# Optimization experiments

Measured on AMD Instinct MI355X. Metric: run time of the kernel, lower is better.

The kernel has to match this reference:

```python
import jax, jax.numpy as jnp
import numpy as np

K = 5       # local window size (odd)
G = 4       # groups

def _gconv1x1(x, w):
    # grouped 1x1 conv: x (b,c,h,w), w (g, c_out_g, c_in_g) -> (b,g,c_out_g,h,w)
    b, c, h, wd = x.shape
    g, co, ci = w.shape
    xg = x.reshape(b, g, ci, h, wd)
    return jnp.einsum('bgihw,goi->bgohw', xg, w)

def _windows(f, h, w):
    # f: (b,g,n,h+2p,w+2p) -> (b,g,n,h,w,K*K), row-major over (ki,kj)
    # matches torch .unfold(2,K,1).unfold(3,K,1).view(..., -1)
    return jnp.stack([f[..., i:i + h, j:j + w]
                      for i in range(K) for j in range(K)], axis=-1)

def setup_inputs() -> dict:
    key = jax.random.key(0)
    k1, k2, k3, k4 = jax.random.split(key, 4)
    x = jax.random.normal(k1, (2, 128, 96, 96), dtype=jnp.float32)
    wq = jax.random.normal(k2, (G, 32, 32), dtype=jnp.float32) * 0.1
    wk = jax.random.normal(k3, (G, 32, 32), dtype=jnp.float32) * 0.1
    wv = jax.random.normal(k4, (G, 32, 32), dtype=jnp.float32) * 0.1
    return {"x": x, "wq": wq, "wk": wk, "wv": wv}

def reference(x, wq, wk, wv):
    b, c, h, w = x.shape
    p = K // 2
    # query: plain grouped 1x1 conv, broadcast over window dim
    q = _gconv1x1(x, wq)[..., None]                      # (b,g,n,h,w,1)
    # key/value: reflect-pad (1x1 conv commutes with padding, same as torch's
    # Conv2d(..., padding=k//2, padding_mode='reflect'))
    xp = jnp.pad(x, ((0, 0), (0, 0), (p, p), (p, p)), mode='reflect')
    kf = _gconv1x1(xp, wk)                               # (b,g,n,h+2p,w+2p)
    vf = _gconv1x1(xp, wv)
    kwin = _windows(kf, h, w)                            # (b,g,n,h,w,K*K)
    vwin = _windows(vf, h, w)
    attn = jax.nn.softmax(q * kwin, axis=-1)             # per-channel window softmax
    y = (attn * vwin).sum(-1)                            # (b,g,n,h,w)
    return y.reshape(b, -1, h, w)                        # (b, c_out, h, w)
```

## Files before the change

### kernel.cpp

```cpp
#include <hip/hip_runtime.h>


#define HW 96
#define RG 12
#define NPOS 144
#define KVSTR 145

typedef short short8 __attribute__((ext_vector_type(8)));
typedef float float4v __attribute__((ext_vector_type(4)));

__device__ __forceinline__ int refl(int i) {
    i = (i < 0) ? -i : i;
    i = (i > 95) ? (190 - i) : i;
    return i;
}

__device__ __forceinline__ unsigned int bfr(float f) {
    return (__float_as_uint(f) + 0x8000u) >> 16;
}

__global__ __launch_bounds__(256) void fused_attn(
    const float* __restrict__ x, const float* __restrict__ wq,
    const float* __restrict__ wk, const float* __restrict__ wv,
    float* __restrict__ out)
{
    __shared__ unsigned short xs[NPOS * 32];
    __shared__ unsigned int   kvb[32 * KVSTR];
    __shared__ unsigned short qs[32 * 64];

    const int tid = threadIdx.x;
    const int g = blockIdx.y, b = blockIdx.z;
    const int h0 = (blockIdx.x / 12) * 8;
    const int w0 = (blockIdx.x % 12) * 8;
    const float* xg = x + (size_t)(b * 128 + g * 32) * (HW * HW);

    const int wA   = min(max(w0 - 4, 0), 80);
    const int colB = wA - w0 + 2;
    #pragma unroll
    for (int it = 0; it < 6; it++) {
        int idx = it * 256 + tid;
        int seg = idx & 3;
        int pr  = idx >> 2;
        int ch  = pr & 31;
        int row = pr >> 5;
        int iy  = refl(h0 + row - 2);
        const float4v f4 = *(const float4v*)(xg + ch * (HW * HW) + iy * HW + wA + seg * 4);
        int col0 = colB + seg * 4;
        #pragma unroll
        for (int e = 0; e < 4; e++) {
            int col = col0 + e;
            if (col >= 0 && col < RG)
                xs[(row * RG + col) * 32 + ch] = (unsigned short)bfr(f4[e]);
        }
    }

    const int wid  = tid >> 6;
    const int lane = tid & 63;
    const int n0   = wid * 8;
    const int col  = lane & 15;
    const int quad = lane >> 4;
    const int koff = quad * 8;

    const float* wrow = (col < 8) ? (wk + (g * 32 + n0 + col) * 32)
                                  : (wv + (g * 32 + n0 + col - 8) * 32);
    short8 bkv;
    #pragma unroll
    for (int j = 0; j < 8; j++)
        ((unsigned short*)&bkv)[j] = (unsigned short)bfr(wrow[koff + j]);

    short8 bq = {0, 0, 0, 0, 0, 0, 0, 0};
    if (col < 8) {
        const float* qr = wq + (g * 32 + n0 + col) * 32;
        #pragma unroll
        for (int j = 0; j < 8; j++)
            ((unsigned short*)&bq)[j] = (unsigned short)bfr(qr[koff + j]);
    }

    if (w0 == 0 || w0 == 88) {
        __syncthreads();
        const int left = (w0 == 0);
        for (int it = 0; it < 3; it++) {
            int idx = it * 256 + tid;
            int ch  = idx & 31;
            int rr  = idx >> 5;
            int row = rr >> 1, wc = rr & 1;
            int dstc = left ? wc : (10 + wc);
            int srcc = left ? (4 - wc) : (8 - wc);
            xs[(row * RG + dstc) * 32 + ch] = xs[(row * RG + srcc) * 32 + ch];
        }
    }
    __syncthreads();

    #pragma unroll
    for (int t = 0; t < 9; t++) {
        int p = t * 16 + col;
        short8 a = *(const short8*)&xs[p * 32 + koff];
        float4v d = {0.f, 0.f, 0.f, 0.f};
        d = __builtin_amdgcn_mfma_f32_16x16x32_bf16(a, bkv, d, 0, 0, 0);
        int c = n0 + (col & 7);
        unsigned short* dst0 = (unsigned short*)&kvb[c * KVSTR + t * 16 + quad * 4];
        int half = (col < 8) ? 0 : 1;
        #pragma unroll
        for (int r = 0; r < 4; r++)
            dst0[2 * r + half] = (unsigned short)bfr(d[r]);
    }

    #pragma unroll
    for (int t = 0; t < 4; t++) {
        int mp = t * 16 + col;
        int p  = ((mp >> 3) + 2) * RG + (mp & 7) + 2;
        short8 a = *(const short8*)&xs[p * 32 + koff];
        float4v d = {0.f, 0.f, 0.f, 0.f};
        d = __builtin_amdgcn_mfma_f32_16x16x32_bf16(a, bq, d, 0, 0, 0);
        if (col < 8) {
            unsigned int* dst = (unsigned int*)&qs[(n0 + col) * 64 + t * 16 + quad * 4];
            unsigned int u0 = __float_as_uint(d[0]) + 0x8000u;
            unsigned int u1 = __float_as_uint(d[1]) + 0x8000u;
            unsigned int u2 = __float_as_uint(d[2]) + 0x8000u;
            unsigned int u3 = __float_as_uint(d[3]) + 0x8000u;
            dst[0] = __builtin_amdgcn_perm(u1, u0, 0x07060302);
            dst[1] = __builtin_amdgcn_perm(u3, u2, 0x07060302);
        }
    }

    __syncthreads();

    const int ty = lane >> 3, tx = lane & 7;
    float* outp = out + (size_t)((b * 128 + g * 32 + n0) * HW + (h0 + ty)) * HW + (w0 + tx);
    for (int n = 0; n < 8; n++) {
        int c = n0 + n;
        float q = __uint_as_float((unsigned int)qs[c * 64 + lane] << 16) * 1.44269504f;
        float den = 0.f, num = 0.f;
        #pragma unroll
        for (int dy = 0; dy < 5; dy++) {
            const unsigned int* rowp = &kvb[c * KVSTR + (ty + dy) * RG + tx];
            #pragma unroll
            for (int dx = 0; dx < 5; dx++) {
                unsigned int u = rowp[dx];
                float kf = __uint_as_float(u << 16);
                float vf = __uint_as_float(u & 0xffff0000u);
                float e;
                asm("v_exp_f32 %0, %1" : "=v"(e) : "v"(q * kf));
                den += e;
                num = fmaf(e, vf, num);
            }
        }
        outp[n * (HW * HW)] = num * __builtin_amdgcn_rcpf(den);
    }
}

extern "C" void kernel_launch(void* const* d_in, const int* in_sizes, int n_in,
                              void* d_out, int out_size, void* d_ws, size_t ws_size,
                              hipStream_t stream) {
    const float* x  = (const float*)d_in[0];
    const float* wq = (const float*)d_in[1];
    const float* wk = (const float*)d_in[2];
    const float* wv = (const float*)d_in[3];
    float* out = (float*)d_out;

    dim3 grid(144, 4, 2);
    fused_attn<<<grid, 256, 0, stream>>>(x, wq, wk, wv, out);
}
```

Measured before the change: 93.61 us.

## Transpose KV shared layout to position-major and process two channels per iteration

```diff
diff --git a/kernel.cpp b/kernel.cpp
--- a/kernel.cpp
+++ b/kernel.cpp
@@ -4,10 +4,16 @@
 #define HW 96
 #define RG 12
 #define NPOS 144
-#define KVSTR 145
+#define CSTR 33
 
 typedef short short8 __attribute__((ext_vector_type(8)));
 typedef float float4v __attribute__((ext_vector_type(4)));
+
+#if __has_builtin(__builtin_amdgcn_exp2f)
+#define EXP2(x) __builtin_amdgcn_exp2f(x)
+#else
+#define EXP2(x) __expf((x) * 0.6931471805599453f)
+#endif
 
 __device__ __forceinline__ int refl(int i) {
     i = (i < 0) ? -i : i;
@@ -25,7 +31,7 @@
     float* __restrict__ out)
 {
     __shared__ unsigned short xs[NPOS * 32];
-    __shared__ unsigned int   kvb[32 * KVSTR];
+    __shared__ unsigned int   kvb[NPOS * CSTR];
     __shared__ unsigned short qs[32 * 64];
 
     const int tid = threadIdx.x;
@@ -91,18 +97,20 @@
     }
     __syncthreads();
 
+    unsigned short* kv16 = (unsigned short*)kvb;
     #pragma unroll
     for (int t = 0; t < 9; t++) {
-        int p = t * 16 + col;
-        short8 a = *(const short8*)&xs[p * 32 + koff];
+        int pa = t * 16 + col;
+        short8 a = *(const short8*)&xs[pa * 32 + koff];
         float4v d = {0.f, 0.f, 0.f, 0.f};
         d = __builtin_amdgcn_mfma_f32_16x16x32_bf16(a, bkv, d, 0, 0, 0);
-        int c = n0 + (col & 7);
-        unsigned short* dst0 = (unsigned short*)&kvb[c * KVSTR + t * 16 + quad * 4];
-        int half = (col < 8) ? 0 : 1;
+        int c    = n0 + (col & 7);
+        int half = col >> 3;
         #pragma unroll
-        for (int r = 0; r < 4; r++)
-            dst0[2 * r + half] = (unsigned short)bfr(d[r]);
+        for (int r = 0; r < 4; r++) {
+            int p = t * 16 + quad * 4 + r;
+            kv16[(p * CSTR + c) * 2 + half] = (unsigned short)bfr(d[r]);
+        }
     }
 
     #pragma unroll
@@ -127,25 +135,32 @@
 
     const int ty = lane >> 3, tx = lane & 7;
     float* outp = out + (size_t)((b * 128 + g * 32 + n0) * HW + (h0 + ty)) * HW + (w0 + tx);
-    for (int n = 0; n < 8; n++) {
-        int c = n0 + n;
-        float q = __uint_as_float((unsigned int)qs[c * 64 + lane] << 16) * 1.44269504f;
-        float den = 0.f, num = 0.f;
+    for (int j = 0; j < 4; j++) {
+        int c0 = n0 + 2 * j;
+        float q0 = __uint_as_float((unsigned int)qs[c0 * 64 + lane] << 16) * 1.44269504f;
+        float q1 = __uint_as_float((unsigned int)qs[(c0 + 1) * 64 + lane] << 16) * 1.44269504f;
+        float den0 = 0.f, num0 = 0.f, den1 = 0.f, num1 = 0.f;
         #pragma unroll
         for (int dy = 0; dy < 5; dy++) {
-            const unsigned int* rowp = &kvb[c * KVSTR + (ty + dy) * RG + tx];
+            const unsigned int* rowp = &kvb[((ty + dy) * RG + tx) * CSTR + c0];
+            float rd0 = 0.f, rn0 = 0.f, rd1 = 0.f, rn1 = 0.f;
             #pragma unroll
             for (int dx = 0; dx < 5; dx++) {
-                unsigned int u = rowp[dx];
-                float kf = __uint_as_float(u << 16);
-                float vf = __uint_as_float(u & 0xffff0000u);
-                float e;
-                asm("v_exp_f32 %0, %1" : "=v"(e) : "v"(q * kf));
-                den += e;
-                num = fmaf(e, vf, num);
+                unsigned int u0 = rowp[dx * CSTR];
+                unsigned int u1 = rowp[dx * CSTR + 1];
+                float k0 = __uint_as_float(u0 << 16);
+                float v0 = __uint_as_float(u0 & 0xffff0000u);
+                float k1 = __uint_as_float(u1 << 16);
+                float v1 = __uint_as_float(u1 & 0xffff0000u);
+                float e0 = EXP2(q0 * k0);
+                float e1 = EXP2(q1 * k1);
+                rd0 += e0; rn0 = fmaf(e0, v0, rn0);
+                rd1 += e1; rn1 = fmaf(e1, v1, rn1);
             }
+            den0 += rd0; num0 += rn0; den1 += rd1; num1 += rn1;
         }
-        outp[n * (HW * HW)] = num * __builtin_amdgcn_rcpf(den);
+        outp[(2 * j)     * (HW * HW)] = num0 * __builtin_amdgcn_rcpf(den0);
+        outp[(2 * j + 1) * (HW * HW)] = num1 * __builtin_amdgcn_rcpf(den1);
     }
 }
 
```

After: 94.86 us. No clear change (+1.3%).

## Switch to fp16 MFMA, channel-innermost K/V layout, vectorized window loads

Applied to the files above, without the earlier changes.

```diff
diff --git a/kernel.cpp b/kernel.cpp
--- a/kernel.cpp
+++ b/kernel.cpp
@@ -4,10 +4,12 @@
 #define HW 96
 #define RG 12
 #define NPOS 144
-#define KVSTR 145
+#define CSTR 36
 
-typedef short short8 __attribute__((ext_vector_type(8)));
-typedef float float4v __attribute__((ext_vector_type(4)));
+typedef _Float16 half8  __attribute__((ext_vector_type(8)));
+typedef _Float16 half2v __attribute__((ext_vector_type(2)));
+typedef float    float4v __attribute__((ext_vector_type(4)));
+typedef unsigned int uint4v __attribute__((ext_vector_type(4)));
 
 __device__ __forceinline__ int refl(int i) {
     i = (i < 0) ? -i : i;
@@ -15,18 +17,15 @@
     return i;
 }
 
-__device__ __forceinline__ unsigned int bfr(float f) {
-    return (__float_as_uint(f) + 0x8000u) >> 16;
-}
-
 __global__ __launch_bounds__(256) void fused_attn(
     const float* __restrict__ x, const float* __restrict__ wq,
     const float* __restrict__ wk, const float* __restrict__ wv,
     float* __restrict__ out)
 {
-    __shared__ unsigned short xs[NPOS * 32];
-    __shared__ unsigned int   kvb[32 * KVSTR];
-    __shared__ unsigned short qs[32 * 64];
+    __shared__ alignas(16) unsigned char smem[9216 + 20736];
+    _Float16*     xs  = (_Float16*)smem;
+    unsigned int* kvb = (unsigned int*)(smem + 9216);
+    _Float16*     qs  = (_Float16*)smem;
 
     const int tid = threadIdx.x;
     const int g = blockIdx.y, b = blockIdx.z;
@@ -50,7 +49,7 @@
         for (int e = 0; e < 4; e++) {
             int col = col0 + e;
             if (col >= 0 && col < RG)
-                xs[(row * RG + col) * 32 + ch] = (unsigned short)bfr(f4[e]);
+                xs[(row * RG + col) * 32 + ch] = (_Float16)f4[e];
         }
     }
 
@@ -63,17 +62,17 @@
 
     const float* wrow = (col < 8) ? (wk + (g * 32 + n0 + col) * 32)
                                   : (wv + (g * 32 + n0 + col - 8) * 32);
-    short8 bkv;
+    half8 bkv;
     #pragma unroll
     for (int j = 0; j < 8; j++)
-        ((unsigned short*)&bkv)[j] = (unsigned short)bfr(wrow[koff + j]);
+        bkv[j] = (_Float16)wrow[koff + j];
 
-    short8 bq = {0, 0, 0, 0, 0, 0, 0, 0};
+    half8 bq = {0, 0, 0, 0, 0, 0, 0, 0};
     if (col < 8) {
         const float* qr = wq + (g * 32 + n0 + col) * 32;
         #pragma unroll
         for (int j = 0; j < 8; j++)
-            ((unsigned short*)&bq)[j] = (unsigned short)bfr(qr[koff + j]);
+            bq[j] = (_Float16)(qr[koff + j] * 1.44269504f);
     }
 
     if (w0 == 0 || w0 == 88) {
@@ -91,62 +90,83 @@
     }
     __syncthreads();
 
+    _Float16* kv16 = (_Float16*)kvb;
     #pragma unroll
     for (int t = 0; t < 9; t++) {
-        int p = t * 16 + col;
-        short8 a = *(const short8*)&xs[p * 32 + koff];
+        int pa = t * 16 + col;
+        half8 a = *(const half8*)&xs[pa * 32 + koff];
         float4v d = {0.f, 0.f, 0.f, 0.f};
-        d = __builtin_amdgcn_mfma_f32_16x16x32_bf16(a, bkv, d, 0, 0, 0);
-        int c = n0 + (col & 7);
-        unsigned short* dst0 = (unsigned short*)&kvb[c * KVSTR + t * 16 + quad * 4];
-        int half = (col < 8) ? 0 : 1;
+        d = __builtin_amdgcn_mfma_f32_16x16x32_f16(a, bkv, d, 0, 0, 0);
+        int c    = n0 + (col & 7);
+        int half_ = col >> 3;
         #pragma unroll
-        for (int r = 0; r < 4; r++)
-            dst0[2 * r + half] = (unsigned short)bfr(d[r]);
+        for (int r = 0; r < 4; r++) {
+            int p = t * 16 + quad * 4 + r;
+            kv16[(p * CSTR + c) * 2 + half_] = (_Float16)d[r];
+        }
     }
 
+    float4v dqv[4];
     #pragma unroll
     for (int t = 0; t < 4; t++) {
         int mp = t * 16 + col;
         int p  = ((mp >> 3) + 2) * RG + (mp & 7) + 2;
-        short8 a = *(const short8*)&xs[p * 32 + koff];
-        float4v d = {0.f, 0.f, 0.f, 0.f};
-        d = __builtin_amdgcn_mfma_f32_16x16x32_bf16(a, bq, d, 0, 0, 0);
-        if (col < 8) {
-            unsigned int* dst = (unsigned int*)&qs[(n0 + col) * 64 + t * 16 + quad * 4];
-            unsigned int u0 = __float_as_uint(d[0]) + 0x8000u;
-            unsigned int u1 = __float_as_uint(d[1]) + 0x8000u;
-            unsigned int u2 = __float_as_uint(d[2]) + 0x8000u;
-            unsigned int u3 = __float_as_uint(d[3]) + 0x8000u;
-            dst[0] = __builtin_amdgcn_perm(u1, u0, 0x07060302);
-            dst[1] = __builtin_amdgcn_perm(u3, u2, 0x07060302);
-        }
+        half8 a = *(const half8*)&xs[p * 32 + koff];
+        float4v z = {0.f, 0.f, 0.f, 0.f};
+        dqv[t] = __builtin_amdgcn_mfma_f32_16x16x32_f16(a, bq, z, 0, 0, 0);
     }
 
     __syncthreads();
 
-    const int ty = lane >> 3, tx = lane & 7;
-    float* outp = out + (size_t)((b * 128 + g * 32 + n0) * HW + (h0 + ty)) * HW + (w0 + tx);
-    for (int n = 0; n < 8; n++) {
-        int c = n0 + n;
-        float q = __uint_as_float((unsigned int)qs[c * 64 + lane] << 16) * 1.44269504f;
-        float den = 0.f, num = 0.f;
+    if (col < 8) {
         #pragma unroll
-        for (int dy = 0; dy < 5; dy++) {
-            const unsigned int* rowp = &kvb[c * KVSTR + (ty + dy) * RG + tx];
+        for (int t = 0; t < 4; t++) {
             #pragma unroll
-            for (int dx = 0; dx < 5; dx++) {
-                unsigned int u = rowp[dx];
-                float kf = __uint_as_float(u << 16);
-                float vf = __uint_as_float(u & 0xffff0000u);
-                float e;
-                asm("v_exp_f32 %0, %1" : "=v"(e) : "v"(q * kf));
-                den += e;
-                num = fmaf(e, vf, num);
+            for (int r = 0; r < 4; r++) {
+                int pix = t * 16 + quad * 4 + r;
+                qs[pix * 32 + n0 + col] = (_Float16)dqv[t][r];
             }
         }
-        outp[n * (HW * HW)] = num * __builtin_amdgcn_rcpf(den);
     }
+    __syncthreads();
+
+    const int ty = lane >> 3, tx = lane & 7;
+
+    half8 qh = *(const half8*)&qs[lane * 32 + n0];
+    float qf[8];
+    #pragma unroll
+    for (int c = 0; c < 8; c++) qf[c] = (float)qh[c];
+
+    float den[8], num[8];
+    #pragma unroll
+    for (int c = 0; c < 8; c++) { den[c] = 0.f; num[c] = 0.f; }
+
+    #pragma unroll
+    for (int dy = 0; dy < 5; dy++) {
+        const unsigned int* base = &kvb[((ty + dy) * RG + tx) * CSTR + n0];
+        uint4v t0[5], t1[5];
+        #pragma unroll
+        for (int dx = 0; dx < 5; dx++) {
+            t0[dx] = *(const uint4v*)(base + dx * CSTR);
+            t1[dx] = *(const uint4v*)(base + dx * CSTR + 4);
+        }
+        #pragma unroll
+        for (int dx = 0; dx < 5; dx++) {
+            #pragma unroll
+            for (int c = 0; c < 8; c++) {
+                unsigned int u = (c < 4) ? t0[dx][c] : t1[dx][c - 4];
+                half2v kv = __builtin_bit_cast(half2v, u);
+                float e = __builtin_amdgcn_exp2f(qf[c] * (float)kv[0]);
+                den[c] += e;
+                num[c] = fmaf(e, (float)kv[1], num[c]);
+            }
+        }
+    }
+
+    float* outp = out + (size_t)((b * 128 + g * 32 + n0) * HW + (h0 + ty)) * HW + (w0 + tx);
+    #pragma unroll
+    for (int c = 0; c < 8; c++)
+        outp[c * (HW * HW)] = num[c] * __builtin_amdgcn_rcpf(den[c]);
 }
 
 extern "C" void kernel_launch(void* const* d_in, const int* in_sizes, int n_in,
```

New measurement: 91.77 us. -2.0%, faster.
